# Performance work log

Hardware: AMD Instinct MI355X
Metric: run time of the kernel (lower is better)

The kernel has to match this reference:

```python
import jax, jax.numpy as jnp
import numpy as np

B, S, DIM, HD = 4, 1024, 2048, 128
H = DIM // HD  # 16 heads
GN_EPS = 1e-3  # Keras GroupNormalization default epsilon


def setup_inputs() -> dict:
    key = jax.random.key(0)
    ks = jax.random.split(key, 8)
    x = jax.random.normal(ks[0], (B, S, DIM), dtype=jnp.float32)
    k = jax.random.normal(ks[1], (B, S, DIM), dtype=jnp.float32)
    v = jax.random.normal(ks[2], (B, S, DIM), dtype=jnp.float32)
    # One shared QKV projection weight per head (dict.fromkeys bug in source
    # makes Q, K, V use the SAME Dense layer). Keras Dense: y = x @ W, W:(in,out)
    Wh = jax.random.normal(ks[3], (H, HD, HD), dtype=jnp.float32) / np.sqrt(HD)
    wg_w = jax.random.normal(ks[4], (DIM, DIM), dtype=jnp.float32) / np.sqrt(DIM)
    wo_w = jax.random.normal(ks[5], (DIM, DIM), dtype=jnp.float32) / np.sqrt(DIM)
    gn_gamma = jnp.ones((DIM,), dtype=jnp.float32)
    gn_beta = jnp.zeros((DIM,), dtype=jnp.float32)
    return {"x": x, "k": k, "v": v, "Wh": Wh, "wg_w": wg_w, "wo_w": wo_w,
            "gn_gamma": gn_gamma, "gn_beta": gn_beta}


def _decay_masks(n_heads, seq_len):
    # Source: band_part(gamma**(i-j), 0, -1) then transpose ->
    # D[h, i, j] = gamma_h ** (j - i) for j <= i, else 0.
    gam = 1.0 - 2.0 ** (-5.0 - jnp.arange(n_heads, dtype=jnp.float32))  # (H,)
    idx = jnp.arange(seq_len, dtype=jnp.float32)
    expo = idx[None, :] - idx[:, None]               # (S,S): j - i
    D = jnp.where(expo[None, :, :] <= 0,
                  gam[:, None, None] ** expo[None, :, :], 0.0)  # (H,S,S)
    # TF: D /= reduce_sum(D, 1)**0.5 broadcasts row-sums along the COLUMN axis
    return D / jnp.sqrt(D.sum(axis=-1))[:, None, :]


def reference(x, k, v, Wh, wg_w, wo_w, gn_gamma, gn_beta):
    b, s, dim = x.shape
    h, hd, _ = Wh.shape
    # split last axis into contiguous per-head chunks
    xh = x.reshape(b, s, h, hd)
    kh = k.reshape(b, s, h, hd)
    vh = v.reshape(b, s, h, hd)
    # Q, K, V share the same per-head weight (faithful to dict.fromkeys)
    Q = jnp.einsum('bshd,hde->bshe', xh, Wh)
    K = jnp.einsum('bshd,hde->bshe', kh, Wh)
    V = jnp.einsum('bshd,hde->bshe', vh, Wh)
    scores = jnp.einsum('bshe,bthe->bhst', Q, K) / jnp.sqrt(jnp.float32(hd))
    Dn = _decay_masks(h, s)                          # (H,S,S)
    masked = scores * Dn[None, :, :, :]              # (B,H,S,S)
    # source reduces over axis 0 == BATCH, then abs, then clamp at 1
    A = jnp.maximum(jnp.abs(masked.sum(axis=0)), 1.0)  # (H,S,S)
    O = jnp.einsum('hst,bthe->bshe', A, V).reshape(b, s, dim)
    # GroupNormalization(groups=1): per-token layernorm over channels
    mu = O.mean(axis=-1, keepdims=True)
    var = O.var(axis=-1, keepdims=True)
    Y = (O - mu) / jnp.sqrt(var + GN_EPS) * gn_gamma + gn_beta
    W = jax.nn.relu(x @ wg_w)                        # gated branch
    return (W * Y) @ wo_w
```

## Files before the change

### kernel.cpp

```cpp
#include <hip/hip_runtime.h>
#include <math.h>

constexpr int Bc = 4, Sc = 1024, Dc = 2048, HDc = 128, Hc = 16;
constexpr int BSc = Bc * Sc;
constexpr int KQKc = Bc * HDc;
#define GN_EPS 1e-3f

typedef __bf16 bf16x8 __attribute__((ext_vector_type(8)));
typedef __bf16 bf16x4 __attribute__((ext_vector_type(4)));
typedef float f32x4 __attribute__((ext_vector_type(4)));

constexpr size_t OFF_Q   = 0;
constexpr size_t OFF_K   = OFF_Q + (size_t)Hc * Sc * KQKc / 2;
constexpr size_t OFF_VB  = OFF_K + (size_t)Hc * Sc * KQKc / 2;
constexpr size_t OFF_VT  = OFF_VB + (size_t)BSc * Dc / 2;
constexpr size_t OFF_A   = OFF_VT + (size_t)BSc * Dc / 2;
constexpr size_t OFF_O   = OFF_A + (size_t)Hc * Sc * Sc / 2;
constexpr size_t OFF_CT  = OFF_O + (size_t)BSc * Dc;
constexpr size_t OFF_PN  = OFF_CT + (size_t)Hc * Sc;
constexpr size_t OFF_XB  = OFF_PN + (size_t)Hc * Sc;
constexpr size_t OFF_WGT = OFF_XB + (size_t)BSc * Dc / 2;
constexpr size_t OFF_WOT = OFF_WGT + (size_t)Dc * Dc / 2;
constexpr size_t OFF_SUF = OFF_WOT + (size_t)Dc * Dc / 2;
constexpr size_t OFF_T   = OFF_SUF + (size_t)64 * 9 * HDc;
constexpr size_t OFF_WHT = OFF_T + (size_t)64 * 8 * HDc;
constexpr size_t OFF_STAT= OFF_WHT + (size_t)Hc * HDc * HDc / 2;
constexpr size_t OFF_KB2 = OFF_A;
constexpr size_t OFF_VB2 = OFF_A + (size_t)BSc * Dc / 2;

#define GLOAD_LDS16(gp, lp)                                               \
  __builtin_amdgcn_global_load_lds(                                       \
      (const __attribute__((address_space(1))) void*)(gp),                \
      (__attribute__((address_space(3))) void*)(lp), 16, 0, 0)


constexpr int ABUFE = 128 * 64;
constexpr int BBUFE = 128 * 64;
constexpr int MG_LDS = (3 * ABUFE + 2 * BBUFE) * 2;
constexpr int PJ_LDS = 4 * 8192 * 2;

template <int ASTR, int BSTR>
__device__ __forceinline__ void mfma_loop128(const __bf16* __restrict__ Abase,
                                             const __bf16* __restrict__ Bbase,
                                             const int ntk,
                                             __bf16* As, __bf16* Bs,
                                             const int wave, const int lane,
                                             f32x4 acc[4][4]) {
  const int wr = wave >> 1, wc = wave & 1;
  const int lr = lane >> 2;
  const int lkx = ((lane & 3) ^ ((lane >> 3) & 3)) * 8;
  const int rl = lane & 15, kq = lane >> 4;
  const int swo = rl * 32 + ((kq ^ ((rl >> 1) & 3)) * 8);

#define SA_(i, kt, bsel) do {                                               \
    const int ci_ = (i) * 4 + wave;                                         \
    GLOAD_LDS16(Abase + (size_t)((ci_ >> 1) * 16 + lr) * ASTR               \
                    + (kt) * 64 + (ci_ & 1) * 32 + lkx,                     \
                As + (bsel) * ABUFE + ci_ * 512);                           \
  } while (0)
#define SB_(j, kt, bsel) do {                                               \
    const int ci_ = (j) * 4 + wave;                                         \
    GLOAD_LDS16(Bbase + (size_t)((ci_ >> 1) * 16 + lr) * BSTR               \
                    + (kt) * 64 + (ci_ & 1) * 32 + lkx,                     \
                Bs + (bsel) * BBUFE + ci_ * 512);                           \
  } while (0)

  SA_(0, 0, 0); SA_(1, 0, 0); SA_(2, 0, 0); SA_(3, 0, 0);
  SB_(0, 0, 0); SB_(1, 0, 0); SB_(2, 0, 0); SB_(3, 0, 0);
  SA_(0, 1, 1); SA_(1, 1, 1); SA_(2, 1, 1); SA_(3, 1, 1);
  __builtin_amdgcn_sched_barrier(0);
  asm volatile("s_waitcnt vmcnt(4)" ::: "memory");
  __builtin_amdgcn_sched_barrier(0);
  __builtin_amdgcn_s_barrier();

  int cbA = 0;
  for (int t = 0; t < ntk; ++t) {
    const int sbA = (cbA + 2 >= 3) ? cbA - 1 : cbA + 2;
    const __bf16* Ac = As + cbA * ABUFE;
    const __bf16* Bc = Bs + (t & 1) * BBUFE;
    bf16x8 a[4][2], b[4][2];
    #pragma unroll
    for (int m = 0; m < 2; ++m)
      #pragma unroll
      for (int kc = 0; kc < 2; ++kc)
        a[m][kc] = *(const bf16x8*)&Ac[((wr * 4 + m) * 2 + kc) * 512 + swo];
    #pragma unroll
    for (int n = 0; n < 2; ++n)
      #pragma unroll
      for (int kc = 0; kc < 2; ++kc)
        b[n][kc] = *(const bf16x8*)&Bc[((wc * 4 + n) * 2 + kc) * 512 + swo];
    #pragma unroll
    for (int m = 2; m < 4; ++m)
      #pragma unroll
      for (int kc = 0; kc < 2; ++kc)
        a[m][kc] = *(const bf16x8*)&Ac[((wr * 4 + m) * 2 + kc) * 512 + swo];
    #pragma unroll
    for (int n = 2; n < 4; ++n)
      #pragma unroll
      for (int kc = 0; kc < 2; ++kc)
        b[n][kc] = *(const bf16x8*)&Bc[((wc * 4 + n) * 2 + kc) * 512 + swo];
    if (t + 1 < ntk) {
      SB_(0, t + 1, (t + 1) & 1); SB_(1, t + 1, (t + 1) & 1);
      SB_(2, t + 1, (t + 1) & 1); SB_(3, t + 1, (t + 1) & 1);
    }
    if (t + 2 < ntk) {
      SA_(0, t + 2, sbA); SA_(1, t + 2, sbA);
      SA_(2, t + 2, sbA); SA_(3, t + 2, sbA);
    }
    __builtin_amdgcn_sched_barrier(0);
    __builtin_amdgcn_s_setprio(1);
    #pragma unroll
    for (int kc = 0; kc < 2; ++kc)
      #pragma unroll
      for (int m = 0; m < 2; ++m)
        #pragma unroll
        for (int n = 0; n < 2; ++n)
          acc[m][n] = __builtin_amdgcn_mfma_f32_16x16x32_bf16(
              a[m][kc], b[n][kc], acc[m][n], 0, 0, 0);
    __builtin_amdgcn_s_setprio(0);
    __builtin_amdgcn_sched_barrier(0);
    __builtin_amdgcn_s_setprio(1);
    #pragma unroll
    for (int kc = 0; kc < 2; ++kc)
      #pragma unroll
      for (int m = 2; m < 4; ++m)
        #pragma unroll
        for (int n = 0; n < 2; ++n)
          acc[m][n] = __builtin_amdgcn_mfma_f32_16x16x32_bf16(
              a[m][kc], b[n][kc], acc[m][n], 0, 0, 0);
    __builtin_amdgcn_s_setprio(0);
    __builtin_amdgcn_sched_barrier(0);
    __builtin_amdgcn_s_setprio(1);
    #pragma unroll
    for (int kc = 0; kc < 2; ++kc)
      #pragma unroll
      for (int m = 0; m < 2; ++m)
        #pragma unroll
        for (int n = 2; n < 4; ++n)
          acc[m][n] = __builtin_amdgcn_mfma_f32_16x16x32_bf16(
              a[m][kc], b[n][kc], acc[m][n], 0, 0, 0);
    __builtin_amdgcn_s_setprio(0);
    __builtin_amdgcn_sched_barrier(0);
    __builtin_amdgcn_s_setprio(1);
    #pragma unroll
    for (int kc = 0; kc < 2; ++kc)
      #pragma unroll
      for (int m = 2; m < 4; ++m)
        #pragma unroll
        for (int n = 2; n < 4; ++n)
          acc[m][n] = __builtin_amdgcn_mfma_f32_16x16x32_bf16(
              a[m][kc], b[n][kc], acc[m][n], 0, 0, 0);
    __builtin_amdgcn_s_setprio(0);
    __builtin_amdgcn_sched_barrier(0);
    asm volatile("s_waitcnt lgkmcnt(0)" ::: "memory");
    __builtin_amdgcn_sched_barrier(0);
    if (t + 2 < ntk)
      asm volatile("s_waitcnt vmcnt(4)" ::: "memory");
    else if (t + 1 < ntk)
      asm volatile("s_waitcnt vmcnt(0)" ::: "memory");
    __builtin_amdgcn_sched_barrier(0);
    __builtin_amdgcn_s_barrier();
    cbA = (cbA + 1 >= 3) ? 0 : cbA + 1;
  }
#undef SA_
#undef SB_
}

__global__ __launch_bounds__(256) void k_tables(float* __restrict__ ct,
                                                float* __restrict__ pn,
                                                float* __restrict__ TP,
                                                float* __restrict__ STAT) {
  int idx = blockIdx.x * 256 + threadIdx.x;
  int h = idx >> 10, t = idx & 1023;
  double gamma = 1.0 - exp2(-(double)(5 + h));
  double l2g = log2(gamma);
  double r = 1.0 / gamma;
  double rowsum = (exp2(-(double)(t + 1) * l2g) - 1.0) / (r - 1.0);
  ct[idx] = (float)(exp2((double)t * l2g) / sqrt(rowsum));
  pn[idx] = (float)exp2(-(double)t * l2g);
  float4 z4 = {0.f, 0.f, 0.f, 0.f};
  *(float4*)(TP + (size_t)idx * 4) = z4;
  if (idx < BSc * 2) STAT[idx] = 0.f;
}

__global__ __launch_bounds__(256) void k_cast83(const float* __restrict__ s0,
                                                const float* __restrict__ s1,
                                                const float* __restrict__ s2,
                                                __bf16* __restrict__ d0,
                                                __bf16* __restrict__ d1,
                                                __bf16* __restrict__ d2) {
  const int y = blockIdx.y;
  const float* src = (y == 0) ? s0 : (y == 1) ? s1 : s2;
  __bf16* dst = (y == 0) ? d0 : (y == 1) ? d1 : d2;
  size_t i = ((size_t)blockIdx.x * 256 + threadIdx.x) * 8;
  float4 a = *(const float4*)(src + i);
  float4 b = *(const float4*)(src + i + 4);
  bf16x8 o;
  o[0] = (__bf16)a.x; o[1] = (__bf16)a.y; o[2] = (__bf16)a.z; o[3] = (__bf16)a.w;
  o[4] = (__bf16)b.x; o[5] = (__bf16)b.y; o[6] = (__bf16)b.z; o[7] = (__bf16)b.w;
  *(bf16x8*)(dst + i) = o;
}

__global__ __launch_bounds__(256) void k_castT2(const float* __restrict__ s0,
                                                const float* __restrict__ s1,
                                                __bf16* __restrict__ d0,
                                                __bf16* __restrict__ d1) {
  __shared__ float t[32][33];
  const int bx = blockIdx.x, by = blockIdx.y;
  const float* src = blockIdx.z ? s1 : s0;
  __bf16* dst = blockIdx.z ? d1 : d0;
  const int tid = threadIdx.x;
  const int lx = tid & 31, ly = tid >> 5;
  #pragma unroll
  for (int r = 0; r < 32; r += 8)
    t[ly + r][lx] = src[(size_t)(by * 32 + ly + r) * Dc + bx * 32 + lx];
  __syncthreads();
  #pragma unroll
  for (int r = 0; r < 32; r += 8)
    dst[(size_t)(bx * 32 + ly + r) * Dc + by * 32 + lx] = (__bf16)t[lx][ly + r];
}

__global__ __launch_bounds__(256) void k_whT(const float* __restrict__ Wh,
                                             __bf16* __restrict__ WhT) {
  __shared__ float t[32][33];
  const int h = blockIdx.z;
  const int d0 = blockIdx.x * 32, e0 = blockIdx.y * 32;
  const int tid = threadIdx.x;
  const int lx = tid & 31, ly = tid >> 5;
  #pragma unroll
  for (int r = 0; r < 32; r += 8)
    t[ly + r][lx] = Wh[(size_t)h * HDc * HDc + (d0 + ly + r) * HDc + e0 + lx];
  __syncthreads();
  #pragma unroll
  for (int r = 0; r < 32; r += 8)
    WhT[(size_t)h * HDc * HDc + (e0 + ly + r) * HDc + d0 + lx] =
        (__bf16)t[lx][ly + r];
}

__global__ __launch_bounds__(256, 2) void k_projm(const __bf16* __restrict__ Xb,
                                                  const __bf16* __restrict__ Kb2,
                                                  const __bf16* __restrict__ Vb2,
                                                  const __bf16* __restrict__ WhT,
                                                  __bf16* __restrict__ Qo,
                                                  __bf16* __restrict__ Ko,
                                                  __bf16* __restrict__ Vo) {
  extern __shared__ __bf16 lds[];
  __bf16* Xs = lds;
  __bf16* Ws = lds + 2 * 8192;
  const int r0 = blockIdx.x * 128;
  const int h = blockIdx.y;
  const int z = blockIdx.z;
  const __bf16* src = (z == 0) ? Xb : (z == 1) ? Kb2 : Vb2;
  const __bf16* wsrc = WhT + (size_t)h * HDc * HDc;
  const int tid = threadIdx.x;
  const int wave = tid >> 6, lane = tid & 63;
  const int wr = wave >> 1, wc = wave & 1;
  const int lr = lane >> 2;
  const int lkx = ((lane & 3) ^ ((lane >> 3) & 3)) * 8;
  const int rl = lane & 15, kq = lane >> 4;
  const int swo = rl * 32 + ((kq ^ ((rl >> 1) & 3)) * 8);
  #pragma unroll
  for (int kt = 0; kt < 2; ++kt) {
    #pragma unroll
    for (int i = 0; i < 4; ++i) {
      const int ci = i * 4 + wave;
      const int row = (ci >> 1) * 16 + lr;
      const int ko = kt * 64 + (ci & 1) * 32 + lkx;
      GLOAD_LDS16(src + (size_t)(r0 + row) * Dc + h * HDc + ko,
                  Xs + kt * 8192 + ci * 512);
      GLOAD_LDS16(wsrc + (size_t)row * HDc + ko, Ws + kt * 8192 + ci * 512);
    }
  }
  __builtin_amdgcn_sched_barrier(0);
  asm volatile("s_waitcnt vmcnt(0)" ::: "memory");
  __builtin_amdgcn_sched_barrier(0);
  __builtin_amdgcn_s_barrier();
  f32x4 acc[4][4] = {{}};
  #pragma unroll
  for (int kt = 0; kt < 2; ++kt) {
    bf16x8 a[4][2], b[4][2];
    #pragma unroll
    for (int m = 0; m < 4; ++m)
      #pragma unroll
      for (int kc = 0; kc < 2; ++kc)
        a[m][kc] =
            *(const bf16x8*)&Xs[kt * 8192 + ((wr * 4 + m) * 2 + kc) * 512 + swo];
    #pragma unroll
    for (int n = 0; n < 4; ++n)
      #pragma unroll
      for (int kc = 0; kc < 2; ++kc)
        b[n][kc] =
            *(const bf16x8*)&Ws[kt * 8192 + ((wc * 4 + n) * 2 + kc) * 512 + swo];
    #pragma unroll
    for (int kc = 0; kc < 2; ++kc)
      #pragma unroll
      for (int m = 0; m < 4; ++m)
        #pragma unroll
        for (int n = 0; n < 4; ++n)
          acc[m][n] = __builtin_amdgcn_mfma_f32_16x16x32_bf16(
              a[m][kc], b[n][kc], acc[m][n], 0, 0, 0);
  }
  #pragma unroll
  for (int mi = 0; mi < 4; ++mi) {
    #pragma unroll
    for (int nj = 0; nj < 4; ++nj) {
      const int col = wc * 64 + nj * 16 + rl;
      #pragma unroll
      for (int r = 0; r < 4; ++r) {
        const int row = r0 + wr * 64 + mi * 16 + kq * 4 + r;
        const __bf16 v = (__bf16)acc[mi][nj][r];
        if (z == 2) {
          Vo[(size_t)row * Dc + h * HDc + col] = v;
        } else {
          const int s = row & 1023, bb = row >> 10;
          __bf16* dst = (z == 0) ? Qo : Ko;
          dst[((size_t)(h * Sc + s) * Bc + bb) * HDc + col] = v;
        }
      }
    }
  }
}

__global__ __launch_bounds__(256) void k_vt(const __bf16* __restrict__ VB,
                                            __bf16* __restrict__ Vt,
                                            float* __restrict__ TP) {
  __shared__ float tl[32][33];
  __shared__ float rs[8][32];
  const int bh = blockIdx.z, bb = bh >> 4, h = bh & 15;
  const int t0 = blockIdx.x * 32, e0 = blockIdx.y * 32;
  const int tid = threadIdx.x;
  const int lx = tid & 31, ly = tid >> 5;
  float ps = 0.f;
  #pragma unroll
  for (int r = 0; r < 32; r += 8) {
    const float v =
        (float)VB[(size_t)(bb * Sc + t0 + ly + r) * Dc + h * HDc + e0 + lx];
    tl[ly + r][lx] = v;
    ps += v;
  }
  rs[ly][lx] = ps;
  __syncthreads();
  #pragma unroll
  for (int r = 0; r < 32; r += 8)
    Vt[((size_t)bh * HDc + e0 + ly + r) * Sc + t0 + lx] = (__bf16)tl[lx][ly + r];
  if (ly == 0) {
    float s = ((rs[0][lx] + rs[1][lx]) + (rs[2][lx] + rs[3][lx])) +
              ((rs[4][lx] + rs[5][lx]) + (rs[6][lx] + rs[7][lx]));
    atomicAdd(&TP[((size_t)bh * 8 + (t0 >> 7)) * HDc + e0 + lx], s);
  }
}

__global__ __launch_bounds__(128) void k_vscan(const float* __restrict__ T,
                                               float* __restrict__ SufV) {
  const int bh = blockIdx.x;
  const int e = threadIdx.x;
  float acc = 0.f;
  SufV[((size_t)bh * 9 + 8) * HDc + e] = 0.f;
  for (int jj = 7; jj >= 1; --jj) {
    acc += T[((size_t)bh * 8 + jj) * HDc + e];
    SufV[((size_t)bh * 9 + jj) * HDc + e] = acc;
  }
}

__global__ __launch_bounds__(256, 2) void k_ssm(const __bf16* __restrict__ Q,
                                                const __bf16* __restrict__ Kb,
                                                const float* __restrict__ ct,
                                                const float* __restrict__ pn,
                                                __bf16* __restrict__ A) {
  const int bx = blockIdx.x, by = blockIdx.y;
  if (bx > by) return;
  extern __shared__ __bf16 lds[];
  __bf16* As = lds;
  __bf16* Bs = lds + 3 * ABUFE;
  const int h = blockIdx.z;
  const int t0 = bx * 128, s0 = by * 128;
  const int tid = threadIdx.x;
  __bf16* Ah = A + (size_t)h * Sc * Sc;
  const int wave = tid >> 6, lane = tid & 63;
  f32x4 acc[4][4] = {{}};
  mfma_loop128<KQKc, KQKc>(Q + (size_t)(h * Sc + s0) * KQKc,
                           Kb + (size_t)(h * Sc + t0) * KQKc, KQKc / 64, As,
                           Bs, wave, lane, acc);
  const int wr = wave >> 1, wc = wave & 1;
  const int rl = lane & 15, kq = lane >> 4;
  const float rs = 0.088388347648318447f;
  #pragma unroll
  for (int mi = 0; mi < 4; ++mi) {
    #pragma unroll
    for (int nj = 0; nj < 4; ++nj) {
      const int t = t0 + wc * 64 + nj * 16 + rl;
      const float ctv = ct[h * Sc + t] * rs;
      #pragma unroll
      for (int r = 0; r < 4; ++r) {
        const int s = s0 + wr * 64 + mi * 16 + kq * 4 + r;
        float v = 1.0f;
        if (t <= s) v = fmaxf(fabsf(ctv * pn[h * Sc + s] * acc[mi][nj][r]), 1.0f);
        Ah[(size_t)s * Sc + t] = (__bf16)v;
      }
    }
  }
}

__global__ __launch_bounds__(256, 2) void k_avm(const __bf16* __restrict__ A,
                                                const __bf16* __restrict__ Vt,
                                                const float* __restrict__ SufV,
                                                float* __restrict__ O,
                                                float* __restrict__ STAT) {
  extern __shared__ __bf16 lds[];
  __bf16* As = lds;
  __bf16* Bs = lds + 3 * ABUFE;
  const int lid = (int)blockIdx.z * 8 + (int)blockIdx.x;
  const int slot = lid & 255;
  const int bh = slot >> 2;
  const int itile = (lid < 256) ? (slot & 3) : 7 - (slot & 3);
  const int bb = bh >> 4, h = bh & 15;
  const int s0 = itile * 128;
  const int tid = threadIdx.x;
  const int wave = tid >> 6, lane = tid & 63;
  const int wr = wave >> 1, wc = wave & 1;
  const int rl = lane & 15, kq = lane >> 4;
  f32x4 acc[4][4] = {{}};
  mfma_loop128<Sc, Sc>(A + (size_t)(h * Sc + s0) * Sc,
                       Vt + (size_t)bh * HDc * Sc, (itile + 1) * 2, As, Bs,
                       wave, lane, acc);
  const float* sufr = SufV + ((size_t)bh * 9 + (itile + 1)) * HDc;
  #pragma unroll
  for (int mi = 0; mi < 4; ++mi) {
    #pragma unroll
    for (int r = 0; r < 4; ++r) {
      const int s = s0 + wr * 64 + mi * 16 + kq * 4 + r;
      const size_t orow = (size_t)(bb * Sc + s);
      float vs = 0.f, vq = 0.f;
      #pragma unroll
      for (int nj = 0; nj < 4; ++nj) {
        const int e = wc * 64 + nj * 16 + rl;
        const float v = acc[mi][nj][r] + sufr[e];
        O[orow * Dc + h * HDc + e] = v;
        vs += v;
        vq += v * v;
      }
      #pragma unroll
      for (int m = 1; m < 16; m <<= 1) {
        vs += __shfl_xor(vs, m);
        vq += __shfl_xor(vq, m);
      }
      if (rl == 0) {
        atomicAdd(&STAT[orow * 2], vs);
        atomicAdd(&STAT[orow * 2 + 1], vq);
      }
    }
  }
}

__global__ __launch_bounds__(256, 2) void k_mgemm(const __bf16* __restrict__ Ab,
                                                  const __bf16* __restrict__ Bt,
                                                  const float* __restrict__ Y,
                                                  const float* __restrict__ gw,
                                                  const float* __restrict__ bw,
                                                  const float* __restrict__ STAT,
                                                  __bf16* __restrict__ Gout,
                                                  float* __restrict__ Fout,
                                                  int mode) {
  extern __shared__ __bf16 lds[];
  __bf16* As = lds;
  __bf16* Bs = lds + 3 * ABUFE;
  int wid = blockIdx.y * gridDim.x + blockIdx.x;
  wid = (wid & 7) * 64 + (wid >> 3);
  const int r0 = (wid >> 4) * 128;
  const int c0 = (wid & 15) * 128;
  const int tid = threadIdx.x;
  const int wave = tid >> 6, lane = tid & 63;
  f32x4 acc[4][4] = {{}};
  mfma_loop128<Dc, Dc>(Ab + (size_t)r0 * Dc, Bt + (size_t)c0 * Dc, Dc / 64,
                       As, Bs, wave, lane, acc);
  const int wr = wave >> 1, wc = wave & 1;
  const int rl = lane & 15, kq = lane >> 4;
  if (mode == 0) {
    #pragma unroll
    for (int mi = 0; mi < 4; ++mi) {
      #pragma unroll
      for (int r = 0; r < 4; ++r) {
        const int row = r0 + wr * 64 + mi * 16 + kq * 4 + r;
        const float mu = STAT[(size_t)row * 2] * (1.0f / Dc);
        const float va = STAT[(size_t)row * 2 + 1] * (1.0f / Dc) - mu * mu;
        const float inv = rsqrtf(va + GN_EPS);
        #pragma unroll
        for (int nj = 0; nj < 4; ++nj) {
          const int col = c0 + wc * 64 + nj * 16 + rl;
          const size_t idx = (size_t)row * Dc + col;
          const float yv = (Y[idx] - mu) * inv * gw[col] + bw[col];
          Gout[idx] = (__bf16)(fmaxf(acc[mi][nj][r], 0.f) * yv);
        }
      }
    }
  } else {
    #pragma unroll
    for (int mi = 0; mi < 4; ++mi) {
      #pragma unroll
      for (int nj = 0; nj < 4; ++nj) {
        const int col = c0 + wc * 64 + nj * 16 + rl;
        #pragma unroll
        for (int r = 0; r < 4; ++r) {
          const int row = r0 + wr * 64 + mi * 16 + kq * 4 + r;
          Fout[(size_t)row * Dc + col] = acc[mi][nj][r];
        }
      }
    }
  }
}

extern "C" void kernel_launch(void* const* d_in, const int* in_sizes, int n_in,
                              void* d_out, int out_size, void* d_ws, size_t ws_size,
                              hipStream_t stream) {
  const float* x  = (const float*)d_in[0];
  const float* k  = (const float*)d_in[1];
  const float* v  = (const float*)d_in[2];
  const float* Wh = (const float*)d_in[3];
  const float* wg = (const float*)d_in[4];
  const float* wo = (const float*)d_in[5];
  const float* gg = (const float*)d_in[6];
  const float* gb = (const float*)d_in[7];
  float* ws = (float*)d_ws;
  __bf16* Q   = (__bf16*)(ws + OFF_Q);
  __bf16* Kp  = (__bf16*)(ws + OFF_K);
  __bf16* VB  = (__bf16*)(ws + OFF_VB);
  __bf16* Vt  = (__bf16*)(ws + OFF_VT);
  __bf16* A   = (__bf16*)(ws + OFF_A);
  float*  O   = ws + OFF_O;
  float*  CT  = ws + OFF_CT;
  float*  PN  = ws + OFF_PN;
  __bf16* XB  = (__bf16*)(ws + OFF_XB);
  __bf16* WGT = (__bf16*)(ws + OFF_WGT);
  __bf16* WOT = (__bf16*)(ws + OFF_WOT);
  float*  SUF = ws + OFF_SUF;
  float*  TP  = ws + OFF_T;
  __bf16* WHT = (__bf16*)(ws + OFF_WHT);
  float*  STAT= ws + OFF_STAT;
  __bf16* KB2 = (__bf16*)(ws + OFF_KB2);
  __bf16* VB2 = (__bf16*)(ws + OFF_VB2);
  __bf16* G   = (__bf16*)(ws + OFF_Q);

  static bool attr_done = false;
  if (!attr_done) {
    (void)hipFuncSetAttribute((const void*)k_mgemm,
                              hipFuncAttributeMaxDynamicSharedMemorySize,
                              MG_LDS);
    (void)hipFuncSetAttribute((const void*)k_projm,
                              hipFuncAttributeMaxDynamicSharedMemorySize,
                              PJ_LDS);
    (void)hipFuncSetAttribute((const void*)k_ssm,
                              hipFuncAttributeMaxDynamicSharedMemorySize,
                              MG_LDS);
    (void)hipFuncSetAttribute((const void*)k_avm,
                              hipFuncAttributeMaxDynamicSharedMemorySize,
                              MG_LDS);
    attr_done = true;
  }

  k_tables<<<Hc * Sc / 256, 256, 0, stream>>>(CT, PN, TP, STAT);
  k_cast83<<<dim3((BSc * Dc) / (256 * 8), 3), 256, 0, stream>>>(
      x, k, v, XB, KB2, VB2);
  k_castT2<<<dim3(Dc / 32, Dc / 32, 2), 256, 0, stream>>>(wg, wo, WGT, WOT);
  k_whT<<<dim3(4, 4, Hc), 256, 0, stream>>>(Wh, WHT);
  k_projm<<<dim3(BSc / 128, Hc, 3), 256, PJ_LDS, stream>>>(XB, KB2, VB2, WHT,
                                                           Q, Kp, VB);
  k_vt<<<dim3(Sc / 32, HDc / 32, Bc * Hc), 256, 0, stream>>>(VB, Vt, TP);
  k_vscan<<<Bc * Hc, 128, 0, stream>>>(TP, SUF);
  k_ssm<<<dim3(Sc / 128, Sc / 128, Hc), 256, MG_LDS, stream>>>(Q, Kp, CT, PN,
                                                               A);
  k_avm<<<dim3(8, 1, Bc * Hc), 256, MG_LDS, stream>>>(A, Vt, SUF, O, STAT);
  k_mgemm<<<dim3(16, 32), 256, MG_LDS, stream>>>(XB, WGT, O, gg, gb, STAT, G,
                                                 nullptr, 0);
  k_mgemm<<<dim3(16, 32), 256, MG_LDS, stream>>>(G, WOT, nullptr, nullptr,
                                                 nullptr, nullptr, nullptr,
                                                 (float*)d_out, 1);
}
```

Before: 356.4 us.

## Rebalance causal score kernel grid into half-width tiles with no idle blocks

The score kernel previously launched a full 8x8 tile grid per head and returned early for upper-triangle blocks. It now maps a 9x8 grid onto 128x64 half tiles of the lower triangle, including the diagonal, so every block computes useful work. The shared MFMA loop gains a template parameter for the number of B fragments. Smaller tiles reduce per-block reuse of the Q tile, but they improve wave balance and tail behaviour.

```diff
diff --git a/kernel.cpp b/kernel.cpp
--- a/kernel.cpp
+++ b/kernel.cpp
@@ -39,13 +39,14 @@
 constexpr int MG_LDS = (3 * ABUFE + 2 * BBUFE) * 2;
 constexpr int PJ_LDS = 4 * 8192 * 2;
 
-template <int ASTR, int BSTR>
+template <int ASTR, int BSTR, int NF = 4>
 __device__ __forceinline__ void mfma_loop128(const __bf16* __restrict__ Abase,
                                              const __bf16* __restrict__ Bbase,
                                              const int ntk,
                                              __bf16* As, __bf16* Bs,
                                              const int wave, const int lane,
                                              f32x4 acc[4][4]) {
+  constexpr int NH = NF / 2;
   const int wr = wave >> 1, wc = wave & 1;
   const int lr = lane >> 2;
   const int lkx = ((lane & 3) ^ ((lane >> 3) & 3)) * 8;
@@ -66,7 +67,8 @@
   } while (0)
 
   SA_(0, 0, 0); SA_(1, 0, 0); SA_(2, 0, 0); SA_(3, 0, 0);
-  SB_(0, 0, 0); SB_(1, 0, 0); SB_(2, 0, 0); SB_(3, 0, 0);
+  #pragma unroll
+  for (int j = 0; j < NF; ++j) SB_(j, 0, 0);
   SA_(0, 1, 1); SA_(1, 1, 1); SA_(2, 1, 1); SA_(3, 1, 1);
   __builtin_amdgcn_sched_barrier(0);
   asm volatile("s_waitcnt vmcnt(4)" ::: "memory");
@@ -78,30 +80,30 @@
     const int sbA = (cbA + 2 >= 3) ? cbA - 1 : cbA + 2;
     const __bf16* Ac = As + cbA * ABUFE;
     const __bf16* Bc = Bs + (t & 1) * BBUFE;
-    bf16x8 a[4][2], b[4][2];
+    bf16x8 a[4][2], b[NF][2];
     #pragma unroll
     for (int m = 0; m < 2; ++m)
       #pragma unroll
       for (int kc = 0; kc < 2; ++kc)
         a[m][kc] = *(const bf16x8*)&Ac[((wr * 4 + m) * 2 + kc) * 512 + swo];
     #pragma unroll
-    for (int n = 0; n < 2; ++n)
+    for (int n = 0; n < NH; ++n)
       #pragma unroll
       for (int kc = 0; kc < 2; ++kc)
-        b[n][kc] = *(const bf16x8*)&Bc[((wc * 4 + n) * 2 + kc) * 512 + swo];
+        b[n][kc] = *(const bf16x8*)&Bc[((wc * NF + n) * 2 + kc) * 512 + swo];
     #pragma unroll
     for (int m = 2; m < 4; ++m)
       #pragma unroll
       for (int kc = 0; kc < 2; ++kc)
         a[m][kc] = *(const bf16x8*)&Ac[((wr * 4 + m) * 2 + kc) * 512 + swo];
     #pragma unroll
-    for (int n = 2; n < 4; ++n)
+    for (int n = NH; n < NF; ++n)
       #pragma unroll
       for (int kc = 0; kc < 2; ++kc)
-        b[n][kc] = *(const bf16x8*)&Bc[((wc * 4 + n) * 2 + kc) * 512 + swo];
+        b[n][kc] = *(const bf16x8*)&Bc[((wc * NF + n) * 2 + kc) * 512 + swo];
     if (t + 1 < ntk) {
-      SB_(0, t + 1, (t + 1) & 1); SB_(1, t + 1, (t + 1) & 1);
-      SB_(2, t + 1, (t + 1) & 1); SB_(3, t + 1, (t + 1) & 1);
+      #pragma unroll
+      for (int j = 0; j < NF; ++j) SB_(j, t + 1, (t + 1) & 1);
     }
     if (t + 2 < ntk) {
       SA_(0, t + 2, sbA); SA_(1, t + 2, sbA);
@@ -114,7 +116,7 @@
       #pragma unroll
       for (int m = 0; m < 2; ++m)
         #pragma unroll
-        for (int n = 0; n < 2; ++n)
+        for (int n = 0; n < NH; ++n)
           acc[m][n] = __builtin_amdgcn_mfma_f32_16x16x32_bf16(
               a[m][kc], b[n][kc], acc[m][n], 0, 0, 0);
     __builtin_amdgcn_s_setprio(0);
@@ -125,7 +127,7 @@
       #pragma unroll
       for (int m = 2; m < 4; ++m)
         #pragma unroll
-        for (int n = 0; n < 2; ++n)
+        for (int n = 0; n < NH; ++n)
           acc[m][n] = __builtin_amdgcn_mfma_f32_16x16x32_bf16(
               a[m][kc], b[n][kc], acc[m][n], 0, 0, 0);
     __builtin_amdgcn_s_setprio(0);
@@ -136,7 +138,7 @@
       #pragma unroll
       for (int m = 0; m < 2; ++m)
         #pragma unroll
-        for (int n = 2; n < 4; ++n)
+        for (int n = NH; n < NF; ++n)
           acc[m][n] = __builtin_amdgcn_mfma_f32_16x16x32_bf16(
               a[m][kc], b[n][kc], acc[m][n], 0, 0, 0);
     __builtin_amdgcn_s_setprio(0);
@@ -147,7 +149,7 @@
       #pragma unroll
       for (int m = 2; m < 4; ++m)
         #pragma unroll
-        for (int n = 2; n < 4; ++n)
+        for (int n = NH; n < NF; ++n)
           acc[m][n] = __builtin_amdgcn_mfma_f32_16x16x32_bf16(
               a[m][kc], b[n][kc], acc[m][n], 0, 0, 0);
     __builtin_amdgcn_s_setprio(0);
@@ -368,33 +370,37 @@
                                                 const float* __restrict__ pn,
                                                 __bf16* __restrict__ A) {
   const int bx = blockIdx.x, by = blockIdx.y;
-  if (bx > by) return;
+  int r, c, half;
+  if (by == 8)       { r = bx; c = bx; half = 1; }
+  else if (bx > by)  { r = bx; c = by; half = 1; }
+  else               { r = by; c = bx; half = 0; }
   extern __shared__ __bf16 lds[];
   __bf16* As = lds;
   __bf16* Bs = lds + 3 * ABUFE;
   const int h = blockIdx.z;
-  const int t0 = bx * 128, s0 = by * 128;
+  const int s0 = r * 128;
+  const int t0 = c * 128 + half * 64;
   const int tid = threadIdx.x;
   __bf16* Ah = A + (size_t)h * Sc * Sc;
   const int wave = tid >> 6, lane = tid & 63;
   f32x4 acc[4][4] = {{}};
-  mfma_loop128<KQKc, KQKc>(Q + (size_t)(h * Sc + s0) * KQKc,
-                           Kb + (size_t)(h * Sc + t0) * KQKc, KQKc / 64, As,
-                           Bs, wave, lane, acc);
+  mfma_loop128<KQKc, KQKc, 2>(Q + (size_t)(h * Sc + s0) * KQKc,
+                              Kb + (size_t)(h * Sc + t0) * KQKc, KQKc / 64,
+                              As, Bs, wave, lane, acc);
   const int wr = wave >> 1, wc = wave & 1;
   const int rl = lane & 15, kq = lane >> 4;
   const float rs = 0.088388347648318447f;
   #pragma unroll
   for (int mi = 0; mi < 4; ++mi) {
     #pragma unroll
-    for (int nj = 0; nj < 4; ++nj) {
-      const int t = t0 + wc * 64 + nj * 16 + rl;
+    for (int nj = 0; nj < 2; ++nj) {
+      const int t = t0 + wc * 32 + nj * 16 + rl;
       const float ctv = ct[h * Sc + t] * rs;
       #pragma unroll
-      for (int r = 0; r < 4; ++r) {
-        const int s = s0 + wr * 64 + mi * 16 + kq * 4 + r;
+      for (int rr = 0; rr < 4; ++rr) {
+        const int s = s0 + wr * 64 + mi * 16 + kq * 4 + rr;
         float v = 1.0f;
-        if (t <= s) v = fmaxf(fabsf(ctv * pn[h * Sc + s] * acc[mi][nj][r]), 1.0f);
+        if (t <= s) v = fmaxf(fabsf(ctv * pn[h * Sc + s] * acc[mi][nj][rr]), 1.0f);
         Ah[(size_t)s * Sc + t] = (__bf16)v;
       }
     }
@@ -566,8 +572,7 @@
                                                            Q, Kp, VB);
   k_vt<<<dim3(Sc / 32, HDc / 32, Bc * Hc), 256, 0, stream>>>(VB, Vt, TP);
   k_vscan<<<Bc * Hc, 128, 0, stream>>>(TP, SUF);
-  k_ssm<<<dim3(Sc / 128, Sc / 128, Hc), 256, MG_LDS, stream>>>(Q, Kp, CT, PN,
-                                                               A);
+  k_ssm<<<dim3(8, 9, Hc), 256, MG_LDS, stream>>>(Q, Kp, CT, PN, A);
   k_avm<<<dim3(8, 1, Bc * Hc), 256, MG_LDS, stream>>>(A, Vt, SUF, O, STAT);
   k_mgemm<<<dim3(16, 32), 256, MG_LDS, stream>>>(XB, WGT, O, gg, gb, STAT, G,
                                                  nullptr, 0);
```

Measured after the change: 348.5 us. 1.02x faster.
